# Kernel optimization log

Measured on AMD Instinct MI355X. Metric: run time of the kernel, lower is better.

## Reference

```python
import jax, jax.numpy as jnp
import numpy as np


def setup_inputs() -> dict:
    key = jax.random.key(0)
    ks = jax.random.split(key, 8)
    B, C, H, W = 16, 256, 64, 64
    E, heads, R = 256, 8, 64
    s = 0.02  # small init scale in lieu of xavier
    return {
        "x": jax.random.normal(ks[0], (B, C, H, W), dtype=jnp.float32),
        "Wqkv": jax.random.normal(ks[1], (3 * E, C), dtype=jnp.float32) * s,
        "bqkv": jnp.zeros((3 * E,), dtype=jnp.float32),
        "Wr": jax.random.normal(ks[2], (2 * R * heads, C), dtype=jnp.float32) * s,
        "br": jnp.zeros((2 * R * heads,), dtype=jnp.float32),
        "Wout": jax.random.normal(ks[3], (C, E), dtype=jnp.float32) * s,
        "bout": jnp.zeros((C,), dtype=jnp.float32),
        "alpha": jax.random.normal(ks[4], (1,), dtype=jnp.float32),
        "num_heads": heads,
        "num_regions": R,
    }


def reference(x, Wqkv, bqkv, Wr, br, Wout, bout, alpha, num_heads, num_regions):
    B, C, H, W = x.shape
    N = H * W
    E = Wqkv.shape[0] // 3
    d = E // num_heads  # head_dim
    xf = x.reshape(B, C, N)  # [B, C, N]

    # qkv 1x1 conv -> [B, 3E, N] -> [B, h, N, 3d] -> q,k,v [B, h, N, d]
    qkv = jnp.einsum("oc,bcn->bon", Wqkv, xf) + bqkv[:, None]
    qkv = qkv.reshape(B, num_heads, 3 * d, N).transpose(0, 1, 3, 2)
    q, k, v = jnp.split(qkv, 3, axis=-1)

    # region projections: 1x1 conv + softmax over the FULL channel axis (2*R*heads)
    r = jnp.einsum("oc,bcn->bon", Wr, xf) + br[:, None]
    r = jax.nn.softmax(r, axis=1)
    r = r.reshape(B, num_heads, 2 * num_regions, N).transpose(0, 1, 3, 2)
    Rq, Rk = jnp.split(r, 2, axis=-1)  # each [B, h, N, R]

    # pool tokens into regions: [B, h, d, R]
    qr = jnp.einsum("bhnd,bhnr->bhdr", q, Rq)
    kr = jnp.einsum("bhnd,bhnr->bhdr", k, Rk)
    vr = jnp.einsum("bhnd,bhnr->bhdr", v, Rk)

    # region-level attention [B, h, Rq, Rk], scaled by sqrt(head_dim)
    logits = jnp.einsum("bhdq,bhdk->bhqk", qr, kr) / jnp.sqrt(jnp.asarray(d, x.dtype))
    attn = jax.nn.softmax(logits, axis=-1)  # dropout is identity at eval

    # values = v_r @ attn^T -> [B, h, d, Rq]; expand back to tokens via Rq^T
    vals = jnp.einsum("bhdk,bhqk->bhdq", vr, attn)
    vals = jnp.einsum("bhdq,bhnq->bhdn", vals, Rq)  # [B, h, d, N]

    vals = vals.reshape(B, E, N)
    out = jnp.einsum("oe,ben->bon", Wout, vals) + bout[:, None]
    out = out.reshape(B, C, H, W)
    return x + alpha * out
```

## Files before the change

kernel.cpp:

```cpp
#include <hip/hip_runtime.h>
#include <cstdint>

typedef unsigned short ushort_t;
typedef __attribute__((ext_vector_type(4))) unsigned short ushort4_t;
typedef __attribute__((ext_vector_type(8))) unsigned short ushort8_t;
typedef __attribute__((ext_vector_type(8))) __bf16 bf16x8;
typedef __attribute__((ext_vector_type(4))) float f32x4;

constexpr int NB = 16;
constexpr int NC = 256;
constexpr int NN = 4096;
constexpr int NP = 1024;
constexpr int NT = 512;
constexpr int NO = 768;

static __device__ __forceinline__ ushort_t f2b(float f) {
  uint32_t u = __builtin_bit_cast(uint32_t, f);
  u += 0x7FFFu + ((u >> 16) & 1u);
  return (ushort_t)(u >> 16);
}
static __device__ __forceinline__ float b2f(ushort_t h) {
  return __builtin_bit_cast(float, (uint32_t)h << 16);
}
static __device__ __forceinline__ f32x4 mfma16(bf16x8 a, bf16x8 b, f32x4 c) {
  return __builtin_amdgcn_mfma_f32_16x16x32_bf16(a, b, c, 0, 0, 0);
}
typedef __attribute__((address_space(1))) const unsigned int guint;
typedef __attribute__((address_space(3))) unsigned int luint;
static __device__ __forceinline__ void glds16(const void* g, void* l) {
  __builtin_amdgcn_global_load_lds((guint*)g, (luint*)l, 16, 0, 0);
}

__global__ __launch_bounds__(256) void k0_cvt(const float* __restrict__ x,
                                              ushort_t* __restrict__ xb,
                                              ushort_t* __restrict__ xt) {
  __shared__ ushort_t tr[64][88];
  const int tid = threadIdx.x;
  const int n0 = blockIdx.x * 64, c0 = blockIdx.y * 64, b = blockIdx.z;
  const int cr = (tid >> 4) * 4;
  const int nc4 = (tid & 15) * 4;
#pragma unroll
  for (int i = 0; i < 4; i++) {
    size_t idx = ((size_t)b * NC + c0 + cr + i) * NN + n0 + nc4;
    float4 v = *(const float4*)(x + idx);
    ushort4_t o;
    o[0] = f2b(v.x); o[1] = f2b(v.y); o[2] = f2b(v.z); o[3] = f2b(v.w);
    *(ushort4_t*)(xb + idx) = o;
    tr[nc4 + 0][cr + i] = o[0];
    tr[nc4 + 1][cr + i] = o[1];
    tr[nc4 + 2][cr + i] = o[2];
    tr[nc4 + 3][cr + i] = o[3];
  }
  __syncthreads();
  const int nr = tid >> 2, cc0 = (tid & 3) * 16;
  size_t odx = ((size_t)b * NN + n0 + nr) * NC + c0 + cc0;
  *(ushort8_t*)(xt + odx) = *(const ushort8_t*)&tr[nr][cc0];
  *(ushort8_t*)(xt + odx + 8) = *(const ushort8_t*)&tr[nr][cc0 + 8];
}

__global__ __launch_bounds__(256) void cvt_f2b_k(const float* __restrict__ src,
                                                 ushort_t* __restrict__ dst) {
  int i = (blockIdx.x * 256 + threadIdx.x) * 4;
  float4 v = *(const float4*)(src + i);
  ushort4_t o;
  o[0] = f2b(v.x); o[1] = f2b(v.y); o[2] = f2b(v.z); o[3] = f2b(v.w);
  *(ushort4_t*)(dst + i) = o;
}

__global__ __launch_bounds__(256) void k1_proj(const ushort_t* __restrict__ Wrb,
                                               const ushort_t* __restrict__ xt,
                                               const float* __restrict__ br,
                                               ushort_t* __restrict__ P) {
  __shared__ __align__(16) ushort_t As[128 * 32];
  __shared__ __align__(16) ushort_t Bs[128 * 32];
  const int tid = threadIdx.x;
  const int ord = blockIdx.x;
  const int L = (ord & 7) * 512 + (ord >> 3);
  const int m0 = (L & 7) * 128;
  const int n0 = ((L >> 3) & 31) * 128;
  const int b = L >> 8;
  const int lane = tid & 63, w = tid >> 6;
  const int wm = (w >> 1) * 64, wn = (w & 1) * 64;
  const int srow = tid >> 2, koff = (tid & 3) * 8;
  ushort_t* A0 = As + w * 512;
  ushort_t* A1 = As + 2048 + w * 512;
  ushort_t* B0 = Bs + w * 512;
  ushort_t* B1 = Bs + 2048 + w * 512;
  const ushort_t* Asrc = Wrb + (size_t)(m0 + srow) * NC + koff;
  const ushort_t* Bsrc = xt + ((size_t)b * NN + n0 + srow) * NC + koff;
  f32x4 acc[4][4] = {};
  const int fr = lane & 15, kq = (lane >> 4) * 8;
  for (int k0 = 0; k0 < NC; k0 += 32) {
    glds16(Asrc + k0, A0);
    glds16(Asrc + (size_t)64 * NC + k0, A1);
    glds16(Bsrc + k0, B0);
    glds16(Bsrc + (size_t)64 * NC + k0, B1);
    __syncthreads();
    bf16x8 af[4], bf[4];
#pragma unroll
    for (int f = 0; f < 4; f++) {
      af[f] = *(const bf16x8*)&As[(wm + f * 16 + fr) * 32 + kq];
      bf[f] = *(const bf16x8*)&Bs[(wn + f * 16 + fr) * 32 + kq];
    }
#pragma unroll
    for (int fm = 0; fm < 4; fm++)
#pragma unroll
      for (int fn = 0; fn < 4; fn++) acc[fm][fn] = mfma16(af[fm], bf[fn], acc[fm][fn]);
    __syncthreads();
  }
  const int col = lane & 15, rb = (lane >> 4) * 4;
#pragma unroll
  for (int fm = 0; fm < 4; fm++)
#pragma unroll
    for (int rg = 0; rg < 4; rg++) {
      int row = m0 + wm + fm * 16 + rb + rg;
      float bias = br[row];
#pragma unroll
      for (int fn = 0; fn < 4; fn++) {
        int cc = n0 + wn + fn * 16 + col;
        P[((size_t)b * NP + row) * NN + cc] = f2b(acc[fm][fn][rg] + bias);
      }
    }
}

__global__ __launch_bounds__(512) void k2_softmax(ushort_t* __restrict__ P,
                                                  float* __restrict__ sPpart) {
  __shared__ float red[64][64];
  __shared__ float Mf[64], If[64];
  const int tid = threadIdx.x;
  const int n0 = blockIdx.x * 64, b = blockIdx.y;
  const int cg = tid & 7, pg = tid >> 3;
  ushort_t* base = P + (size_t)b * NP * NN + n0 + cg * 8;

  ushort8_t v[16];
  float m[8];
#pragma unroll
  for (int j = 0; j < 8; j++) m[j] = -3.0e38f;
#pragma unroll
  for (int r = 0; r < 16; r++) {
    v[r] = *(const ushort8_t*)(base + (size_t)(pg * 16 + r) * NN);
#pragma unroll
    for (int j = 0; j < 8; j++) m[j] = fmaxf(m[j], b2f(v[r][j]));
  }
#pragma unroll
  for (int j = 0; j < 8; j++) red[pg][cg * 8 + j] = m[j];
  __syncthreads();
  if (tid < 64) {
    float M = -3.0e38f;
    for (int g = 0; g < 64; g++) M = fmaxf(M, red[g][tid]);
    Mf[tid] = M;
  }
  __syncthreads();
  float mj[8], s[8];
#pragma unroll
  for (int j = 0; j < 8; j++) { mj[j] = Mf[cg * 8 + j]; s[j] = 0.f; }
#pragma unroll
  for (int r = 0; r < 16; r++)
#pragma unroll
    for (int j = 0; j < 8; j++) s[j] += __expf(b2f(v[r][j]) - mj[j]);
#pragma unroll
  for (int j = 0; j < 8; j++) red[pg][cg * 8 + j] = s[j];
  __syncthreads();
  if (tid < 64) {
    float S = 0.f;
    for (int g = 0; g < 64; g++) S += red[g][tid];
    If[tid] = 1.f / S;
  }
  __syncthreads();
  float ij[8];
#pragma unroll
  for (int j = 0; j < 8; j++) ij[j] = If[cg * 8 + j];
#pragma unroll
  for (int r = 0; r < 16; r++) {
    int p = pg * 16 + r;
    ushort8_t o;
    float rs = 0.f;
#pragma unroll
    for (int j = 0; j < 8; j++) {
      float e = __expf(b2f(v[r][j]) - mj[j]) * ij[j];
      o[j] = f2b(e);
      rs += e;
    }
    *(ushort8_t*)(base + (size_t)p * NN) = o;
    rs += __shfl_xor(rs, 1, 64);
    rs += __shfl_xor(rs, 2, 64);
    rs += __shfl_xor(rs, 4, 64);
    if (cg == 0) sPpart[((size_t)blockIdx.x * NB + b) * NP + p] = rs;
  }
}

__global__ __launch_bounds__(256) void k2r_reduce(const float* __restrict__ sPpart,
                                                  float* __restrict__ sP) {
  int idx = blockIdx.x * 256 + threadIdx.x;
  float s = 0.f;
#pragma unroll 8
  for (int bx = 0; bx < 64; bx++) s += sPpart[(size_t)bx * (NB * NP) + idx];
  sP[idx] = s;
}

__global__ __launch_bounds__(256) void k3_pool(const ushort_t* __restrict__ xb,
                                               const ushort_t* __restrict__ P,
                                               float* __restrict__ XR4) {
  __shared__ __align__(16) ushort_t As[128 * 32];
  __shared__ __align__(16) ushort_t Bs[128 * 32];
  const int tid = threadIdx.x;
  const int ord = blockIdx.x;
  const int L = (ord & 7) * 64 + (ord >> 3);
  const int m0 = (L & 1) * 128;
  const int n0 = ((L >> 1) & 7) * 128;
  const int zz = L >> 4;
  const int b = zz >> 1, ks = zz & 1;
  const int lane = tid & 63, w = tid >> 6;
  const int wm = (w >> 1) * 64, wn = (w & 1) * 64;
  const int srow = tid >> 2, koff = (tid & 3) * 8;
  ushort_t* A0 = As + w * 512;
  ushort_t* A1 = As + 2048 + w * 512;
  ushort_t* B0 = Bs + w * 512;
  ushort_t* B1 = Bs + 2048 + w * 512;
  const ushort_t* Asrc = xb + ((size_t)b * NC + m0 + srow) * NN + koff;
  const ushort_t* Bsrc = P + ((size_t)b * NP + n0 + srow) * NN + koff;
  f32x4 acc[4][4] = {};
  const int fr = lane & 15, kq = (lane >> 4) * 8;
  const int kbeg = ks * 2048, kend = kbeg + 2048;
  for (int k0 = kbeg; k0 < kend; k0 += 32) {
    glds16(Asrc + k0, A0);
    glds16(Asrc + (size_t)64 * NN + k0, A1);
    glds16(Bsrc + k0, B0);
    glds16(Bsrc + (size_t)64 * NN + k0, B1);
    __syncthreads();
    bf16x8 af[4], bf[4];
#pragma unroll
    for (int f = 0; f < 4; f++) {
      af[f] = *(const bf16x8*)&As[(wm + f * 16 + fr) * 32 + kq];
      bf[f] = *(const bf16x8*)&Bs[(wn + f * 16 + fr) * 32 + kq];
    }
#pragma unroll
    for (int fm = 0; fm < 4; fm++)
#pragma unroll
      for (int fn = 0; fn < 4; fn++) acc[fm][fn] = mfma16(af[fm], bf[fn], acc[fm][fn]);
    __syncthreads();
  }
  const int col = lane & 15, rb = (lane >> 4) * 4;
  float* outp = XR4 + (size_t)(ks * NB + b) * NC * NP;
#pragma unroll
  for (int fm = 0; fm < 4; fm++)
#pragma unroll
    for (int fn = 0; fn < 4; fn++)
#pragma unroll
      for (int rg = 0; rg < 4; rg++) {
        int row = m0 + wm + fm * 16 + rb + rg;
        int cc = n0 + wn + fn * 16 + col;
        outp[(size_t)row * NP + cc] = acc[fm][fn][rg];
      }
}

__global__ __launch_bounds__(256) void k3r_tr(const float* __restrict__ XR4,
                                              ushort_t* __restrict__ XRbT) {
  __shared__ ushort_t tr[64][72];
  const int tid = threadIdx.x;
  const int p0 = blockIdx.x * 64, c0 = blockIdx.y * 64, b = blockIdx.z;
  const size_t slice = (size_t)NB * NC * NP;
  const int row = tid >> 4, col4 = (tid & 15) * 4;
#pragma unroll
  for (int i = 0; i < 4; i++) {
    int c = row + i * 16;
    size_t idx = ((size_t)b * NC + c0 + c) * NP + p0 + col4;
    float4 v0 = *(const float4*)(XR4 + idx);
    float4 v1 = *(const float4*)(XR4 + idx + slice);
    tr[col4 + 0][c] = f2b(v0.x + v1.x);
    tr[col4 + 1][c] = f2b(v0.y + v1.y);
    tr[col4 + 2][c] = f2b(v0.z + v1.z);
    tr[col4 + 3][c] = f2b(v0.w + v1.w);
  }
  __syncthreads();
  const int prow = tid >> 2, coff = (tid & 3) * 16;
  size_t odx = ((size_t)b * NP + p0 + prow) * NC + c0 + coff;
  *(ushort8_t*)(XRbT + odx) = *(const ushort8_t*)&tr[prow][coff];
  *(ushort8_t*)(XRbT + odx + 8) = *(const ushort8_t*)&tr[prow][coff + 8];
}

__global__ __launch_bounds__(256) void k4a_qkvr(const ushort_t* __restrict__ Wqkvb,
                                                const ushort_t* __restrict__ XRbT,
                                                const float* __restrict__ bqkv,
                                                const float* __restrict__ sP,
                                                ushort_t* __restrict__ QKVRb) {
  __shared__ __align__(16) ushort_t As[128 * 32];
  __shared__ __align__(16) ushort_t Bs[128 * 32];
  const int tid = threadIdx.x;
  const int ord = blockIdx.x;
  const int L = (ord & 7) * 96 + (ord >> 3);
  const int m0 = (L % 6) * 128;
  const int rest = L / 6;
  const int n0 = (rest & 7) * 128;
  const int b = rest >> 3;
  const int lane = tid & 63, w = tid >> 6;
  const int wm = (w >> 1) * 64, wn = (w & 1) * 64;
  const int srow = tid >> 2, koff = (tid & 3) * 8;
  ushort_t* A0 = As + w * 512;
  ushort_t* A1 = As + 2048 + w * 512;
  ushort_t* B0 = Bs + w * 512;
  ushort_t* B1 = Bs + 2048 + w * 512;
  const ushort_t* Asrc = Wqkvb + (size_t)(m0 + srow) * NC + koff;
  const ushort_t* Bsrc = XRbT + ((size_t)b * NP + n0 + srow) * NC + koff;
  f32x4 acc[4][4] = {};
  const int fr = lane & 15, kq = (lane >> 4) * 8;
  for (int k0 = 0; k0 < NC; k0 += 32) {
    glds16(Asrc + k0, A0);
    glds16(Asrc + (size_t)64 * NC + k0, A1);
    glds16(Bsrc + k0, B0);
    glds16(Bsrc + (size_t)64 * NC + k0, B1);
    __syncthreads();
    bf16x8 af[4], bf[4];
#pragma unroll
    for (int f = 0; f < 4; f++) {
      af[f] = *(const bf16x8*)&As[(wm + f * 16 + fr) * 32 + kq];
      bf[f] = *(const bf16x8*)&Bs[(wn + f * 16 + fr) * 32 + kq];
    }
#pragma unroll
    for (int fm = 0; fm < 4; fm++)
#pragma unroll
      for (int fn = 0; fn < 4; fn++) acc[fm][fn] = mfma16(af[fm], bf[fn], acc[fm][fn]);
    __syncthreads();
  }
  const int col = lane & 15, rb = (lane >> 4) * 4;
  float spv[4];
#pragma unroll
  for (int fn = 0; fn < 4; fn++) spv[fn] = sP[(size_t)b * NP + n0 + wn + fn * 16 + col];
#pragma unroll
  for (int fm = 0; fm < 4; fm++)
#pragma unroll
    for (int rg = 0; rg < 4; rg++) {
      int row = m0 + wm + fm * 16 + rb + rg;
      float bq = bqkv[row];
#pragma unroll
      for (int fn = 0; fn < 4; fn++) {
        int cc = n0 + wn + fn * 16 + col;
        QKVRb[((size_t)b * NO + row) * NP + cc] = f2b(acc[fm][fn][rg] + bq * spv[fn]);
      }
    }
}

__global__ __launch_bounds__(256) void k4b_attn(const ushort_t* __restrict__ QKVRb,
                                                const float* __restrict__ Wout,
                                                ushort_t* __restrict__ Tmb) {
  const int b = blockIdx.x >> 3, h = blockIdx.x & 7;
  const int tid = threadIdx.x;
  __shared__ float qf[96][64];
  __shared__ float attn_sT[64][65];
  __shared__ float vals_s[32][64];
#pragma unroll
  for (int i = 0; i < 3; i++) {
    int u = i * 256 + tid;
    int rw = u >> 3, jc = (u & 7) * 8;
    int p0 = h * 128 + ((rw < 32) ? 0 : 64);
    ushort8_t v = *(const ushort8_t*)(QKVRb + ((size_t)b * NO + h * 96 + rw) * NP + p0 + jc);
#pragma unroll
    for (int j = 0; j < 8; j++) qf[rw][jc + j] = b2f(v[j]);
  }
  __syncthreads();
  const int lj = tid & 63;
  const int rq = tid >> 6;
  float kcol[32];
#pragma unroll
  for (int dd = 0; dd < 32; dd++) kcol[dd] = qf[32 + dd][lj];
  const float isc = 0.17677669529663687f;
#pragma unroll
  for (int r = 0; r < 16; r++) {
    int qi = r * 4 + rq;
    float a = 0.f;
#pragma unroll
    for (int dd = 0; dd < 32; dd++) a += qf[dd][qi] * kcol[dd];
    attn_sT[lj][qi] = a * isc;
  }
  __syncthreads();
  if (tid < 64) {
    float m = -3e38f;
    for (int k = 0; k < 64; k++) m = fmaxf(m, attn_sT[k][tid]);
    float s = 0.f;
    for (int k = 0; k < 64; k++) {
      float e = __expf(attn_sT[k][tid] - m);
      attn_sT[k][tid] = e;
      s += e;
    }
    float inv = 1.f / s;
    for (int k = 0; k < 64; k++) attn_sT[k][tid] *= inv;
  }
  __syncthreads();
  float acol[64];
#pragma unroll
  for (int k = 0; k < 64; k++) acol[k] = attn_sT[k][lj];
#pragma unroll
  for (int r = 0; r < 8; r++) {
    int dd = r * 4 + rq;
    float a = 0.f;
#pragma unroll
    for (int k = 0; k < 64; k++) a += qf[64 + dd][k] * acol[k];
    vals_s[dd][lj] = a;
  }
  __syncthreads();
  float vcol[32];
#pragma unroll
  for (int dd = 0; dd < 32; dd++) vcol[dd] = vals_s[dd][lj];
  for (int r = 0; r < 64; r++) {
    int c = r * 4 + rq;
    const float4* wp = (const float4*)(Wout + (size_t)c * NC + h * 32);
    float a = 0.f;
#pragma unroll
    for (int t = 0; t < 8; t++) {
      float4 w = wp[t];
      a += w.x * vcol[t * 4] + w.y * vcol[t * 4 + 1] + w.z * vcol[t * 4 + 2] +
           w.w * vcol[t * 4 + 3];
    }
    Tmb[((size_t)b * NC + c) * NT + h * 64 + lj] = f2b(a);
  }
}

__global__ __launch_bounds__(256) void k5_out(const float* __restrict__ x,
                                              const ushort_t* __restrict__ P,
                                              const ushort_t* __restrict__ Tmb,
                                              const float* __restrict__ bout,
                                              const float* __restrict__ alpha,
                                              float* __restrict__ out) {
  __shared__ __align__(16) ushort_t As[128 * 32];
  __shared__ __align__(16) ushort_t Bs[128 * 40];
  const int tid = threadIdx.x;
  const int ord = blockIdx.x;
  const int L = (ord & 7) * 128 + (ord >> 3);
  const int m0 = (L & 1) * 128;
  const int n0 = ((L >> 1) & 31) * 128;
  const int b = L >> 6;
  const int lane = tid & 63, w = tid >> 6;
  const int wm = (w >> 1) * 64, wn = (w & 1) * 64;
  const int srow = tid >> 2, koff = (tid & 3) * 8;
  ushort_t* A0 = As + w * 512;
  ushort_t* A1 = As + 2048 + w * 512;
  const ushort_t* Asrc = Tmb + ((size_t)b * NC + m0 + srow) * NT + koff;
  const int kg = tid >> 5, ng = (tid & 31) * 4;
  f32x4 acc[4][4] = {};
  const int fr = lane & 15, kq = (lane >> 4) * 8;
  for (int k0 = 0; k0 < NT; k0 += 32) {
    glds16(Asrc + k0, A0);
    glds16(Asrc + (size_t)64 * NT + k0, A1);
#pragma unroll
    for (int i = 0; i < 4; i++) {
      int hj = k0 + kg * 4 + i;
      int prow = ((hj >> 6) << 7) + (hj & 63);
      ushort4_t v = *(const ushort4_t*)(P + ((size_t)b * NP + prow) * NN + n0 + ng);
#pragma unroll
      for (int jj = 0; jj < 4; jj++) Bs[(ng + jj) * 40 + kg * 4 + i] = v[jj];
    }
    __syncthreads();
    bf16x8 af[4], bf[4];
#pragma unroll
    for (int f = 0; f < 4; f++) {
      af[f] = *(const bf16x8*)&As[(wm + f * 16 + fr) * 32 + kq];
      bf[f] = *(const bf16x8*)&Bs[(wn + f * 16 + fr) * 40 + kq];
    }
#pragma unroll
    for (int fm = 0; fm < 4; fm++)
#pragma unroll
      for (int fn = 0; fn < 4; fn++) acc[fm][fn] = mfma16(af[fm], bf[fn], acc[fm][fn]);
    __syncthreads();
  }
  const float al = alpha[0];
  const int col = lane & 15, rb = (lane >> 4) * 4;
#pragma unroll
  for (int fm = 0; fm < 4; fm++)
#pragma unroll
    for (int rg = 0; rg < 4; rg++) {
      int row = m0 + wm + fm * 16 + rb + rg;
      float bias = bout[row];
#pragma unroll
      for (int fn = 0; fn < 4; fn++) {
        int cc = n0 + wn + fn * 16 + col;
        size_t idx = ((size_t)b * NC + row) * NN + cc;
        out[idx] = x[idx] + al * (acc[fm][fn][rg] + bias);
      }
    }
}

extern "C" void kernel_launch(void* const* d_in, const int* in_sizes, int n_in,
                              void* d_out, int out_size, void* d_ws, size_t ws_size,
                              hipStream_t stream) {
  const float* x = (const float*)d_in[0];
  const float* Wqkv = (const float*)d_in[1];
  const float* bqkv = (const float*)d_in[2];
  const float* Wr = (const float*)d_in[3];
  const float* br = (const float*)d_in[4];
  const float* Wout = (const float*)d_in[5];
  const float* bout = (const float*)d_in[6];
  const float* alpha = (const float*)d_in[7];
  float* out = (float*)d_out;

  char* ws = (char*)d_ws;
  ushort_t* P = (ushort_t*)ws;
  ushort_t* xb = (ushort_t*)(ws + 134217728);
  ushort_t* XRbT = (ushort_t*)(ws + 134217728);
  ushort_t* xt = (ushort_t*)(ws + 167772160);
  float* XR4 = (float*)(ws + 167772160);
  ushort_t* QKVRb = (ushort_t*)(ws + 167772160);
  ushort_t* Wrb = (ushort_t*)(ws + 201326592);
  float* sPpart = (float*)(ws + 201850880);
  ushort_t* Wqkvb = (ushort_t*)(ws + 201850880);
  float* sP = (float*)(ws + 206045184);
  ushort_t* Tmb = (ushort_t*)(ws + 206110720);

  k0_cvt<<<dim3(64, 4, 16), 256, 0, stream>>>(x, xb, xt);
  cvt_f2b_k<<<256, 256, 0, stream>>>(Wr, Wrb);
  k1_proj<<<4096, 256, 0, stream>>>(Wrb, xt, br, P);
  k2_softmax<<<dim3(64, 16), 512, 0, stream>>>(P, sPpart);
  k2r_reduce<<<64, 256, 0, stream>>>(sPpart, sP);
  cvt_f2b_k<<<192, 256, 0, stream>>>(Wqkv, Wqkvb);
  k3_pool<<<512, 256, 0, stream>>>(xb, P, XR4);
  k3r_tr<<<dim3(16, 4, 16), 256, 0, stream>>>(XR4, XRbT);
  k4a_qkvr<<<768, 256, 0, stream>>>(Wqkvb, XRbT, bqkv, sP, QKVRb);
  k4b_attn<<<128, 256, 0, stream>>>(QKVRb, Wout, Tmb);
  k5_out<<<1024, 256, 0, stream>>>(x, P, Tmb, bout, alpha, out);
}
```

Measured before the change: 334.7 us.

## Widen GEMM K-tile to 64 with XOR-swizzled LDS and shared gemm core

Factors the four MFMA GEMM kernels' main loops into a templated gemm_core that stages 64-wide K tiles, halving the number of barrier pairs per K. LDS rows are XOR-swizzled at load and read time to avoid bank conflicts on the wider rows. k5_out also uses 64-wide K steps and packs the transposed P values into 16-byte LDS stores instead of scalar stores. This doubles LDS use per block, which may lower occupancy.

```diff
diff --git a/kernel.cpp b/kernel.cpp
--- a/kernel.cpp
+++ b/kernel.cpp
@@ -29,6 +29,46 @@
 typedef __attribute__((address_space(3))) unsigned int luint;
 static __device__ __forceinline__ void glds16(const void* g, void* l) {
   __builtin_amdgcn_global_load_lds((guint*)g, (luint*)l, 16, 0, 0);
+}
+
+template <int KITERS>
+__device__ __forceinline__ void gemm_core(const ushort_t* __restrict__ Asrc, size_t lda,
+                                          const ushort_t* __restrict__ Bsrc, size_t ldb,
+                                          ushort_t* As, ushort_t* Bs,
+                                          f32x4 (&acc)[4][4], int tid) {
+  const int l = tid & 63, w = tid >> 6;
+  const int fr = l & 15, kq = (l >> 4) * 8;
+  const int rr = l >> 3;
+  const int sc = ((l & 7) ^ rr) << 3;
+  const int swz = (fr & 7) << 3;
+  const int wm = (w >> 1) * 64, wn = (w & 1) * 64;
+#pragma unroll 1
+  for (int it = 0; it < KITERS; it++) {
+    const size_t k0 = (size_t)it * 64;
+#pragma unroll
+    for (int i = 0; i < 4; i++) {
+      const int row = i * 32 + w * 8 + rr;
+      glds16(Asrc + (size_t)row * lda + k0 + sc, As + (i * 32 + w * 8) * 64);
+      glds16(Bsrc + (size_t)row * ldb + k0 + sc, Bs + (i * 32 + w * 8) * 64);
+    }
+    __syncthreads();
+#pragma unroll
+    for (int ks = 0; ks < 2; ks++) {
+      const int col = ks * 32 + kq;
+      bf16x8 af[4], bf[4];
+#pragma unroll
+      for (int f = 0; f < 4; f++) {
+        af[f] = *(const bf16x8*)&As[(wm + f * 16 + fr) * 64 + (col ^ swz)];
+        bf[f] = *(const bf16x8*)&Bs[(wn + f * 16 + fr) * 64 + (col ^ swz)];
+      }
+#pragma unroll
+      for (int fm = 0; fm < 4; fm++)
+#pragma unroll
+        for (int fn = 0; fn < 4; fn++)
+          acc[fm][fn] = mfma16(af[fm], bf[fn], acc[fm][fn]);
+    }
+    __syncthreads();
+  }
 }
 
 __global__ __launch_bounds__(256) void k0_cvt(const float* __restrict__ x,
@@ -71,8 +111,8 @@
                                                const ushort_t* __restrict__ xt,
                                                const float* __restrict__ br,
                                                ushort_t* __restrict__ P) {
-  __shared__ __align__(16) ushort_t As[128 * 32];
-  __shared__ __align__(16) ushort_t Bs[128 * 32];
+  __shared__ __align__(16) ushort_t As[128 * 64];
+  __shared__ __align__(16) ushort_t Bs[128 * 64];
   const int tid = threadIdx.x;
   const int ord = blockIdx.x;
   const int L = (ord & 7) * 512 + (ord >> 3);
@@ -81,33 +121,9 @@
   const int b = L >> 8;
   const int lane = tid & 63, w = tid >> 6;
   const int wm = (w >> 1) * 64, wn = (w & 1) * 64;
-  const int srow = tid >> 2, koff = (tid & 3) * 8;
-  ushort_t* A0 = As + w * 512;
-  ushort_t* A1 = As + 2048 + w * 512;
-  ushort_t* B0 = Bs + w * 512;
-  ushort_t* B1 = Bs + 2048 + w * 512;
-  const ushort_t* Asrc = Wrb + (size_t)(m0 + srow) * NC + koff;
-  const ushort_t* Bsrc = xt + ((size_t)b * NN + n0 + srow) * NC + koff;
   f32x4 acc[4][4] = {};
-  const int fr = lane & 15, kq = (lane >> 4) * 8;
-  for (int k0 = 0; k0 < NC; k0 += 32) {
-    glds16(Asrc + k0, A0);
-    glds16(Asrc + (size_t)64 * NC + k0, A1);
-    glds16(Bsrc + k0, B0);
-    glds16(Bsrc + (size_t)64 * NC + k0, B1);
-    __syncthreads();
-    bf16x8 af[4], bf[4];
-#pragma unroll
-    for (int f = 0; f < 4; f++) {
-      af[f] = *(const bf16x8*)&As[(wm + f * 16 + fr) * 32 + kq];
-      bf[f] = *(const bf16x8*)&Bs[(wn + f * 16 + fr) * 32 + kq];
-    }
-#pragma unroll
-    for (int fm = 0; fm < 4; fm++)
-#pragma unroll
-      for (int fn = 0; fn < 4; fn++) acc[fm][fn] = mfma16(af[fm], bf[fn], acc[fm][fn]);
-    __syncthreads();
-  }
+  gemm_core<4>(Wrb + (size_t)m0 * NC, NC,
+               xt + ((size_t)b * NN + n0) * NC, NC, As, Bs, acc, tid);
   const int col = lane & 15, rb = (lane >> 4) * 4;
 #pragma unroll
   for (int fm = 0; fm < 4; fm++)
@@ -201,8 +217,8 @@
 __global__ __launch_bounds__(256) void k3_pool(const ushort_t* __restrict__ xb,
                                                const ushort_t* __restrict__ P,
                                                float* __restrict__ XR4) {
-  __shared__ __align__(16) ushort_t As[128 * 32];
-  __shared__ __align__(16) ushort_t Bs[128 * 32];
+  __shared__ __align__(16) ushort_t As[128 * 64];
+  __shared__ __align__(16) ushort_t Bs[128 * 64];
   const int tid = threadIdx.x;
   const int ord = blockIdx.x;
   const int L = (ord & 7) * 64 + (ord >> 3);
@@ -212,34 +228,10 @@
   const int b = zz >> 1, ks = zz & 1;
   const int lane = tid & 63, w = tid >> 6;
   const int wm = (w >> 1) * 64, wn = (w & 1) * 64;
-  const int srow = tid >> 2, koff = (tid & 3) * 8;
-  ushort_t* A0 = As + w * 512;
-  ushort_t* A1 = As + 2048 + w * 512;
-  ushort_t* B0 = Bs + w * 512;
-  ushort_t* B1 = Bs + 2048 + w * 512;
-  const ushort_t* Asrc = xb + ((size_t)b * NC + m0 + srow) * NN + koff;
-  const ushort_t* Bsrc = P + ((size_t)b * NP + n0 + srow) * NN + koff;
   f32x4 acc[4][4] = {};
-  const int fr = lane & 15, kq = (lane >> 4) * 8;
-  const int kbeg = ks * 2048, kend = kbeg + 2048;
-  for (int k0 = kbeg; k0 < kend; k0 += 32) {
-    glds16(Asrc + k0, A0);
-    glds16(Asrc + (size_t)64 * NN + k0, A1);
-    glds16(Bsrc + k0, B0);
-    glds16(Bsrc + (size_t)64 * NN + k0, B1);
-    __syncthreads();
-    bf16x8 af[4], bf[4];
-#pragma unroll
-    for (int f = 0; f < 4; f++) {
-      af[f] = *(const bf16x8*)&As[(wm + f * 16 + fr) * 32 + kq];
-      bf[f] = *(const bf16x8*)&Bs[(wn + f * 16 + fr) * 32 + kq];
-    }
-#pragma unroll
-    for (int fm = 0; fm < 4; fm++)
-#pragma unroll
-      for (int fn = 0; fn < 4; fn++) acc[fm][fn] = mfma16(af[fm], bf[fn], acc[fm][fn]);
-    __syncthreads();
-  }
+  const size_t kbeg = (size_t)ks * 2048;
+  gemm_core<32>(xb + ((size_t)b * NC + m0) * NN + kbeg, NN,
+                P + ((size_t)b * NP + n0) * NN + kbeg, NN, As, Bs, acc, tid);
   const int col = lane & 15, rb = (lane >> 4) * 4;
   float* outp = XR4 + (size_t)(ks * NB + b) * NC * NP;
 #pragma unroll
@@ -284,8 +276,8 @@
                                                 const float* __restrict__ bqkv,
                                                 const float* __restrict__ sP,
                                                 ushort_t* __restrict__ QKVRb) {
-  __shared__ __align__(16) ushort_t As[128 * 32];
-  __shared__ __align__(16) ushort_t Bs[128 * 32];
+  __shared__ __align__(16) ushort_t As[128 * 64];
+  __shared__ __align__(16) ushort_t Bs[128 * 64];
   const int tid = threadIdx.x;
   const int ord = blockIdx.x;
   const int L = (ord & 7) * 96 + (ord >> 3);
@@ -295,33 +287,9 @@
   const int b = rest >> 3;
   const int lane = tid & 63, w = tid >> 6;
   const int wm = (w >> 1) * 64, wn = (w & 1) * 64;
-  const int srow = tid >> 2, koff = (tid & 3) * 8;
-  ushort_t* A0 = As + w * 512;
-  ushort_t* A1 = As + 2048 + w * 512;
-  ushort_t* B0 = Bs + w * 512;
-  ushort_t* B1 = Bs + 2048 + w * 512;
-  const ushort_t* Asrc = Wqkvb + (size_t)(m0 + srow) * NC + koff;
-  const ushort_t* Bsrc = XRbT + ((size_t)b * NP + n0 + srow) * NC + koff;
   f32x4 acc[4][4] = {};
-  const int fr = lane & 15, kq = (lane >> 4) * 8;
-  for (int k0 = 0; k0 < NC; k0 += 32) {
-    glds16(Asrc + k0, A0);
-    glds16(Asrc + (size_t)64 * NC + k0, A1);
-    glds16(Bsrc + k0, B0);
-    glds16(Bsrc + (size_t)64 * NC + k0, B1);
-    __syncthreads();
-    bf16x8 af[4], bf[4];
-#pragma unroll
-    for (int f = 0; f < 4; f++) {
-      af[f] = *(const bf16x8*)&As[(wm + f * 16 + fr) * 32 + kq];
-      bf[f] = *(const bf16x8*)&Bs[(wn + f * 16 + fr) * 32 + kq];
-    }
-#pragma unroll
-    for (int fm = 0; fm < 4; fm++)
-#pragma unroll
-      for (int fn = 0; fn < 4; fn++) acc[fm][fn] = mfma16(af[fm], bf[fn], acc[fm][fn]);
-    __syncthreads();
-  }
+  gemm_core<4>(Wqkvb + (size_t)m0 * NC, NC,
+               XRbT + ((size_t)b * NP + n0) * NC, NC, As, Bs, acc, tid);
   const int col = lane & 15, rb = (lane >> 4) * 4;
   float spv[4];
 #pragma unroll
@@ -421,8 +389,8 @@
                                               const float* __restrict__ bout,
                                               const float* __restrict__ alpha,
                                               float* __restrict__ out) {
-  __shared__ __align__(16) ushort_t As[128 * 32];
-  __shared__ __align__(16) ushort_t Bs[128 * 40];
+  __shared__ __align__(16) ushort_t As[128 * 64];
+  __shared__ __align__(16) ushort_t Bs[128 * 72];
   const int tid = threadIdx.x;
   const int ord = blockIdx.x;
   const int L = (ord & 7) * 128 + (ord >> 3);
@@ -431,35 +399,48 @@
   const int b = L >> 6;
   const int lane = tid & 63, w = tid >> 6;
   const int wm = (w >> 1) * 64, wn = (w & 1) * 64;
-  const int srow = tid >> 2, koff = (tid & 3) * 8;
-  ushort_t* A0 = As + w * 512;
-  ushort_t* A1 = As + 2048 + w * 512;
-  const ushort_t* Asrc = Tmb + ((size_t)b * NC + m0 + srow) * NT + koff;
+  const int fr = lane & 15, kq = (lane >> 4) * 8;
+  const int rr = lane >> 3, sc = ((lane & 7) ^ rr) << 3;
+  const int swz = (fr & 7) << 3;
+  const ushort_t* Asrc = Tmb + ((size_t)b * NC + m0) * NT;
   const int kg = tid >> 5, ng = (tid & 31) * 4;
   f32x4 acc[4][4] = {};
-  const int fr = lane & 15, kq = (lane >> 4) * 8;
-  for (int k0 = 0; k0 < NT; k0 += 32) {
-    glds16(Asrc + k0, A0);
-    glds16(Asrc + (size_t)64 * NT + k0, A1);
+  for (int k0 = 0; k0 < NT; k0 += 64) {
 #pragma unroll
     for (int i = 0; i < 4; i++) {
-      int hj = k0 + kg * 4 + i;
+      const int row = i * 32 + w * 8 + rr;
+      glds16(Asrc + (size_t)row * NT + k0 + sc, As + (i * 32 + w * 8) * 64);
+    }
+    ushort4_t bv[8];
+#pragma unroll
+    for (int i = 0; i < 8; i++) {
+      int hj = k0 + kg * 8 + i;
       int prow = ((hj >> 6) << 7) + (hj & 63);
-      ushort4_t v = *(const ushort4_t*)(P + ((size_t)b * NP + prow) * NN + n0 + ng);
-#pragma unroll
-      for (int jj = 0; jj < 4; jj++) Bs[(ng + jj) * 40 + kg * 4 + i] = v[jj];
+      bv[i] = *(const ushort4_t*)(P + ((size_t)b * NP + prow) * NN + n0 + ng);
+    }
+#pragma unroll
+    for (int jj = 0; jj < 4; jj++) {
+      ushort8_t pk;
+#pragma unroll
+      for (int i = 0; i < 8; i++) pk[i] = bv[i][jj];
+      *(ushort8_t*)&Bs[(ng + jj) * 72 + kg * 8] = pk;
     }
     __syncthreads();
-    bf16x8 af[4], bf[4];
-#pragma unroll
-    for (int f = 0; f < 4; f++) {
-      af[f] = *(const bf16x8*)&As[(wm + f * 16 + fr) * 32 + kq];
-      bf[f] = *(const bf16x8*)&Bs[(wn + f * 16 + fr) * 40 + kq];
-    }
-#pragma unroll
-    for (int fm = 0; fm < 4; fm++)
-#pragma unroll
-      for (int fn = 0; fn < 4; fn++) acc[fm][fn] = mfma16(af[fm], bf[fn], acc[fm][fn]);
+#pragma unroll
+    for (int ks = 0; ks < 2; ks++) {
+      const int col = ks * 32 + kq;
+      bf16x8 af[4], bf[4];
+#pragma unroll
+      for (int f = 0; f < 4; f++) {
+        af[f] = *(const bf16x8*)&As[(wm + f * 16 + fr) * 64 + (col ^ swz)];
+        bf[f] = *(const bf16x8*)&Bs[(wn + f * 16 + fr) * 72 + col];
+      }
+#pragma unroll
+      for (int fm = 0; fm < 4; fm++)
+#pragma unroll
+        for (int fn = 0; fn < 4; fn++)
+          acc[fm][fn] = mfma16(af[fm], bf[fn], acc[fm][fn]);
+    }
     __syncthreads();
   }
   const float al = alpha[0];
```

Measured after the change: 337.8 us. No clear change (+0.9%).
